# Kernel tuning notes

Hardware: AMD Instinct MI355X
Metric: run time of the kernel (lower is better)

Reference implementation:

```python
import jax, jax.numpy as jnp
import numpy as np

K_T, K_H, K_W = 3, 3, 3
STRIDE = (1, 1, 1)
PAD = (1, 1, 1)
DIL = (1, 1, 1)


def setup_inputs() -> dict:
    key = jax.random.key(0)
    k1, k2, k3, k4 = jax.random.split(key, 4)
    B, C, T, H, W = 2, 16, 8, 64, 64
    Co = 16
    K = K_T * K_H * K_W  # 27
    x = jax.random.normal(k1, (B, C, T, H, W), jnp.float32)
    temp = jax.random.normal(k2, (B, 2 * K, T, H, W), jnp.float32)
    weight = jax.random.normal(k3, (Co, C, K_T, K_H, K_W), jnp.float32) * 0.05
    bias = jax.random.normal(k4, (Co,), jnp.float32) * 0.05
    return {"x": x, "temp": temp, "weight": weight, "bias": bias}


def _build_offset_hw(temp):
    # dimension='HW': per kernel location, offset = (0, temp[2i], temp[2i+1])
    B, c2, T, H, W = temp.shape
    K = c2 // 2
    t = temp.reshape(B, K, 2, T, H, W)
    zeros = jnp.zeros((B, K, 1, T, H, W), temp.dtype)
    return jnp.concatenate([zeros, t], axis=2)  # [B, K, 3, T, H, W]


def _deform_conv3d(x, off, weight, bias):
    # x: [B,C,T,H,W]; off: [B,K,3,To,Ho,Wo]; weight: [Co,C,kT,kH,kW]
    B, C, T, H, W = x.shape
    Co = weight.shape[0]
    K = K_T * K_H * K_W
    st, sh, sw = STRIDE
    pt, ph, pw = PAD
    dt, dh, dw = DIL
    To = (T + 2 * pt - dt * (K_T - 1) - 1) // st + 1
    Ho = (H + 2 * ph - dh * (K_H - 1) - 1) // sh + 1
    Wo = (W + 2 * pw - dw * (K_W - 1) - 1) // sw + 1
    # kernel tap coordinates, flattened to [K]
    kt, kh, kw = jnp.meshgrid(jnp.arange(K_T) * dt, jnp.arange(K_H) * dh,
                              jnp.arange(K_W) * dw, indexing='ij')
    kt, kh, kw = kt.ravel(), kh.ravel(), kw.ravel()
    # base sampling grid (top-left-front corner of receptive field)
    bt = (jnp.arange(To) * st - pt).astype(x.dtype)
    bh = (jnp.arange(Ho) * sh - ph).astype(x.dtype)
    bw = (jnp.arange(Wo) * sw - pw).astype(x.dtype)
    # fractional sampling positions, each [B,K,To,Ho,Wo]
    p_t = bt[None, None, :, None, None] + kt[None, :, None, None, None].astype(x.dtype) + off[:, :, 0]
    p_h = bh[None, None, None, :, None] + kh[None, :, None, None, None].astype(x.dtype) + off[:, :, 1]
    p_w = bw[None, None, None, None, :] + kw[None, :, None, None, None].astype(x.dtype) + off[:, :, 2]
    t0 = jnp.floor(p_t); h0 = jnp.floor(p_h); w0 = jnp.floor(p_w)
    ft = p_t - t0; fh = p_h - h0; fw = p_w - w0
    t0 = t0.astype(jnp.int32); h0 = h0.astype(jnp.int32); w0 = w0.astype(jnp.int32)
    x_flat = x.reshape(B, C, T * H * W)

    def gather_one(xf, idx):  # xf: [C, THW], idx: [K,To,Ho,Wo]
        return xf[:, idx.ravel()].reshape((C,) + idx.shape)

    gather = jax.vmap(gather_one)  # over batch

    val = jnp.zeros((B, C, K, To, Ho, Wo), x.dtype)
    for ot in (0, 1):
        wt = ft if ot else (1.0 - ft)
        ti = t0 + ot
        for oh in (0, 1):
            wh = fh if oh else (1.0 - fh)
            hi = h0 + oh
            for ow in (0, 1):
                ww = fw if ow else (1.0 - fw)
                wi = w0 + ow
                valid = ((ti >= 0) & (ti < T) & (hi >= 0) & (hi < H)
                         & (wi >= 0) & (wi < W))
                idx = (jnp.clip(ti, 0, T - 1) * (H * W)
                       + jnp.clip(hi, 0, H - 1) * W
                       + jnp.clip(wi, 0, W - 1))
                g = gather(x_flat, idx)  # [B,C,K,To,Ho,Wo]
                coef = (wt * wh * ww) * valid.astype(x.dtype)
                val = val + g * coef[:, None]
    w2 = weight.reshape(Co, C, K)
    out = jnp.einsum('bcktuv,ock->botuv', val, w2)
    return out + bias[None, :, None, None, None]


def reference(x, temp, weight, bias):
    off = _build_offset_hw(temp)
    return _deform_conv3d(x, off, weight, bias)
```

## Files before the change

### kernel.cpp

```cpp
#include <hip/hip_runtime.h>

#define BB 2
#define CC 16
#define TT 8
#define HH 64
#define WW 64
#define CO 16
#define KK 27
#define THW (TT*HH*WW)
#define HW  (HH*WW)

typedef _Float16 h8   __attribute__((ext_vector_type(8)));
typedef _Float16 h16  __attribute__((ext_vector_type(16)));
typedef int      i4   __attribute__((ext_vector_type(4)));
typedef float    f32x2 __attribute__((ext_vector_type(2)));

__global__ __launch_bounds__(256) void prep(const float* __restrict__ x,
                                            const float* __restrict__ w,
                                            _Float16* __restrict__ xT,
                                            float* __restrict__ wT) {
    int bid = blockIdx.x;
    if (bid < 256) {
        int pos = bid * 256 + threadIdx.x;
        int b = pos / THW;
        int s = pos - b * THW;
        h16 hv;
#pragma unroll
        for (int c = 0; c < CC; ++c)
            hv[c] = (_Float16)x[(size_t)(b * CC + c) * THW + s];
        *(h16*)(xT + (size_t)pos * CC) = hv;
    } else {
        int id = (bid - 256) * 256 + threadIdx.x;
        if (id < KK * CC * CO) {
            int k  = id / (CC * CO);
            int c  = (id / CO) % CC;
            int co = id % CO;
            wT[id] = w[(size_t)(co * CC + c) * KK + k];
        }
    }
}

template <int CTRL>
__device__ __forceinline__ h8 dppq(h8 v) {
    i4 sv = __builtin_bit_cast(i4, v);
    i4 d;
#pragma unroll
    for (int j = 0; j < 4; ++j)
        d[j] = __builtin_amdgcn_mov_dpp(sv[j], CTRL, 0xF, 0xF, true);
    return __builtin_bit_cast(h8, d);
}

__global__ __launch_bounds__(512, 4) void deform_pair(
    const _Float16* __restrict__ xT, const float* __restrict__ temp,
    const float* __restrict__ wT, const float* __restrict__ bias,
    float* __restrict__ out)
{
    __shared__ float red[4 * CO * 64];

    int tid = threadIdx.x;
    int e   = tid & 1;
    int wl  = (tid >> 1) & 31;
    int wh  = __builtin_amdgcn_readfirstlane((tid >> 6) & 1);
    int g   = __builtin_amdgcn_readfirstlane(tid >> 7);
    int w   = wh * 32 + wl;
    int s0  = blockIdx.x * 64;
    int b   = s0 / THW;
    int sb  = s0 - b * THW;
    int t   = sb / HW;
    int h   = (sb - t * HW) >> 6;

    const float* tb = temp + (size_t)b * (2 * KK) * THW + sb + w;
    float offh[7], offw[7];
#pragma unroll
    for (int i = 0; i < 7; ++i) {
        int k = g + 4 * i;
        if (k < KK) {
            offh[i] = tb[(size_t)(2 * k)     * THW];
            offw[i] = tb[(size_t)(2 * k + 1) * THW];
        }
    }

    f32x2 acc2[8];
#pragma unroll
    for (int j = 0; j < 8; ++j) acc2[j] = f32x2{0.f, 0.f};

#pragma unroll
    for (int i = 0; i < 7; ++i) {
        int k = g + 4 * i;
        if (k >= KK) continue;
        int kt = k / 9, kh = (k / 3) % 3, kw = k % 3;
        int pt = t - 1 + kt;
        if (pt < 0 || pt >= TT) continue;

        float ph = (float)(h - 1 + kh) + offh[i];
        float pw = (float)(w - 1 + kw) + offw[i];
        float r0f = floorf(ph), w0f = floorf(pw);
        float fh = ph - r0f, fw = pw - w0f;
        int r0 = (int)r0f, w0i = (int)w0f;
        int r1 = r0 + 1, w1i = w0i + 1;
        bool vh0 = (unsigned)r0  < (unsigned)HH;
        bool vh1 = (unsigned)r1  < (unsigned)HH;
        bool vw0 = (unsigned)w0i < (unsigned)WW;
        bool vw1 = (unsigned)w1i < (unsigned)WW;
        float fh1 = 1.f - fh, fw1 = 1.f - fw;
        float c00 = fh1 * fw1 * ((vh0 && vw0) ? 1.f : 0.f);
        float c01 = fh1 * fw  * ((vh0 && vw1) ? 1.f : 0.f);
        float c10 = fh  * fw1 * ((vh1 && vw0) ? 1.f : 0.f);
        float c11 = fh  * fw  * ((vh1 && vw1) ? 1.f : 0.f);
        int cc0 = min(max(w0i, 0), WW - 1);
        int cc1 = min(max(w1i, 0), WW - 1);
        int rr0 = min(max(r0, 0), HH - 1);
        int rr1 = min(max(r1, 0), HH - 1);

        const _Float16* xb = xT + (size_t)((b * TT + pt) * HW) * CC + e * 8;
        h8 q00 = *(const h8*)(xb + (size_t)(rr0 * WW + cc0) * CC);
        h8 q01 = *(const h8*)(xb + (size_t)(rr0 * WW + cc1) * CC);
        h8 q10 = *(const h8*)(xb + (size_t)(rr1 * WW + cc0) * CC);
        h8 q11 = *(const h8*)(xb + (size_t)(rr1 * WW + cc1) * CC);

        h8 va = q00 * (_Float16)c00 + q01 * (_Float16)c01
              + q10 * (_Float16)c10 + q11 * (_Float16)c11;

        h8 vlow  = dppq<0xA0>(va);
        h8 vhigh = dppq<0xF5>(va);

        const f32x2* wk = (const f32x2*)(wT + k * (CC * CO));
#pragma unroll
        for (int c = 0; c < 8; ++c) {
            float vl = (float)vlow[c];
            float vh = (float)vhigh[c];
#pragma unroll
            for (int jj = 0; jj < 8; ++jj) {
                acc2[jj] += wk[c * 8 + jj] * vl;
                acc2[jj] += wk[(c + 8) * 8 + jj] * vh;
            }
        }
    }

    if (e == 0) {
#pragma unroll
        for (int j = 0; j < 8; ++j) {
            red[g * (CO * 64) + (2 * j)     * 64 + w] = acc2[j][0];
            red[g * (CO * 64) + (2 * j + 1) * 64 + w] = acc2[j][1];
        }
    }
    __syncthreads();

#pragma unroll
    for (int rep = 0; rep < 2; ++rep) {
        int idx = tid + rep * 512;
        int co = idx >> 6, pp = idx & 63;
        float sum = red[             co * 64 + pp]
                  + red[1 * CO * 64 + co * 64 + pp]
                  + red[2 * CO * 64 + co * 64 + pp]
                  + red[3 * CO * 64 + co * 64 + pp] + bias[co];
        out[(size_t)b * CO * THW + (size_t)co * THW + sb + pp] = sum;
    }
}

__global__ __launch_bounds__(256) void deform_global(
    const float* __restrict__ x, const float* __restrict__ temp,
    const float* __restrict__ weight, const float* __restrict__ bias,
    float* __restrict__ out)
{
    int pos = blockIdx.x * 256 + threadIdx.x;
    int b = pos / THW, s = pos - b * THW;
    int t = s / HW, hw = s - t * HW, h = hw >> 6, w = hw & 63;
    float acc[CO];
#pragma unroll
    for (int co = 0; co < CO; ++co) acc[co] = bias[co];
#pragma unroll 1
    for (int k = 0; k < KK; ++k) {
        int kt = k / 9, kh = (k / 3) % 3, kw = k % 3;
        int pt = t - 1 + kt;
        if (pt < 0 || pt >= TT) continue;
        const float* tb = temp + (size_t)b * (2 * KK) * THW + s;
        float ph = (float)(h - 1 + kh) + tb[(size_t)(2 * k) * THW];
        float pw = (float)(w - 1 + kw) + tb[(size_t)(2 * k + 1) * THW];
        float h0f = floorf(ph), w0f = floorf(pw);
        float fh = ph - h0f, fw = pw - w0f;
        int h0 = (int)h0f, w0 = (int)w0f;
        float val[CC];
#pragma unroll
        for (int c = 0; c < CC; ++c) val[c] = 0.f;
#pragma unroll
        for (int dh = 0; dh < 2; ++dh) {
            int hi = h0 + dh;
            float whf = dh ? fh : (1.f - fh);
            bool vh = (hi >= 0) && (hi < HH);
            int hic = min(max(hi, 0), HH - 1);
#pragma unroll
            for (int dw_ = 0; dw_ < 2; ++dw_) {
                int wi = w0 + dw_;
                float wwf = dw_ ? fw : (1.f - fw);
                bool vw = (wi >= 0) && (wi < WW);
                int wic = min(max(wi, 0), WW - 1);
                float coef = whf * wwf * ((vh && vw) ? 1.f : 0.f);
                const float* xp = x + (size_t)(b * CC) * THW + pt * HW
                                + hic * WW + wic;
#pragma unroll
                for (int c = 0; c < CC; ++c)
                    val[c] = fmaf(coef, xp[(size_t)c * THW], val[c]);
            }
        }
#pragma unroll
        for (int c = 0; c < CC; ++c)
#pragma unroll
            for (int co = 0; co < CO; ++co)
                acc[co] = fmaf(val[c], weight[(size_t)(co * CC + c) * KK + k],
                               acc[co]);
    }
#pragma unroll
    for (int co = 0; co < CO; ++co)
        out[(size_t)(b * CO + co) * THW + s] = acc[co];
}

extern "C" void kernel_launch(void* const* d_in, const int* in_sizes, int n_in,
                              void* d_out, int out_size, void* d_ws, size_t ws_size,
                              hipStream_t stream) {
    const float* x      = (const float*)d_in[0];
    const float* temp   = (const float*)d_in[1];
    const float* weight = (const float*)d_in[2];
    const float* bias   = (const float*)d_in[3];
    float* out = (float*)d_out;

    const size_t xT_bytes = (size_t)BB * THW * CC * sizeof(_Float16);
    const size_t wT_bytes = (size_t)KK * CC * CO * sizeof(float);

    if (ws_size >= xT_bytes + wT_bytes) {
        _Float16* xT = (_Float16*)d_ws;
        float*    wT = (float*)((char*)d_ws + xT_bytes);
        hipLaunchKernelGGL(prep, dim3(256 + 27), dim3(256), 0, stream,
                           x, weight, xT, wT);
        hipLaunchKernelGGL(deform_pair, dim3((BB * THW) / 64), dim3(512),
                           0, stream, xT, temp, wT, bias, out);
    } else {
        hipLaunchKernelGGL(deform_global, dim3((BB * THW) / 256), dim3(256),
                           0, stream, x, temp, weight, bias, out);
    }
}
```

Baseline: 97.80 us.

## Stage input halo tile in swizzled LDS for bilinear gathers

Each block now handles two output rows and first loads a 3-frame by 13-row halo of the fp16 channels-last input into shared memory, using an XOR swizzle to reduce bank conflicts. The four bilinear corner reads then come from LDS, with a rare global fallback when an offset lands outside the staged rows. Each thread now reads all 16 channels itself, so the DPP lane exchange between thread pairs is gone. The aim is to replace scattered global/L2 gathers with LDS reads, at the cost of about 78KB of LDS per block, which limits occupancy, plus extra staging work.

```diff
diff --git a/kernel.cpp b/kernel.cpp
--- a/kernel.cpp
+++ b/kernel.cpp
@@ -12,8 +12,11 @@
 
 typedef _Float16 h8   __attribute__((ext_vector_type(8)));
 typedef _Float16 h16  __attribute__((ext_vector_type(16)));
-typedef int      i4   __attribute__((ext_vector_type(4)));
 typedef float    f32x2 __attribute__((ext_vector_type(2)));
+
+#define NROW 13
+#define ROWB 2048
+#define TILEB (3 * NROW * ROWB)
 
 __global__ __launch_bounds__(256) void prep(const float* __restrict__ x,
                                             const float* __restrict__ w,
@@ -40,36 +43,36 @@
     }
 }
 
-template <int CTRL>
-__device__ __forceinline__ h8 dppq(h8 v) {
-    i4 sv = __builtin_bit_cast(i4, v);
-    i4 d;
-#pragma unroll
-    for (int j = 0; j < 4; ++j)
-        d[j] = __builtin_amdgcn_mov_dpp(sv[j], CTRL, 0xF, 0xF, true);
-    return __builtin_bit_cast(h8, d);
-}
-
-__global__ __launch_bounds__(512, 4) void deform_pair(
+__device__ __forceinline__ int swz(int rr, int c, int base) {
+    int sw = ((((c >> 2) ^ rr) & 3) << 4) | (((c >> 4) & 1) << 6);
+    return base ^ sw;
+}
+
+__global__ __launch_bounds__(512, 4) void deform_lds2(
     const _Float16* __restrict__ xT, const float* __restrict__ temp,
     const float* __restrict__ wT, const float* __restrict__ bias,
     float* __restrict__ out)
 {
-    __shared__ float red[4 * CO * 64];
+    __shared__ __align__(16) char lds[TILEB];
 
     int tid = threadIdx.x;
-    int e   = tid & 1;
-    int wl  = (tid >> 1) & 31;
-    int wh  = __builtin_amdgcn_readfirstlane((tid >> 6) & 1);
-    int g   = __builtin_amdgcn_readfirstlane(tid >> 7);
-    int w   = wh * 32 + wl;
-    int s0  = blockIdx.x * 64;
-    int b   = s0 / THW;
-    int sb  = s0 - b * THW;
-    int t   = sb / HW;
-    int h   = (sb - t * HW) >> 6;
-
-    const float* tb = temp + (size_t)b * (2 * KK) * THW + sb + w;
+    int lane = tid & 63;
+    int wid  = __builtin_amdgcn_readfirstlane(tid >> 6);
+    int row  = wid >> 2;
+    int g    = wid & 3;
+    int blk = blockIdx.x;
+    int b   = blk >> 8;
+    int rem = blk & 255;
+    int t   = rem >> 5;
+    int h0  = (rem & 31) * 2;
+    int rlo = max(0, h0 - 5);
+    int rhi = min(HH - 1, h0 + 7);
+
+    int h = h0 + row;
+    int w = lane;
+    const float* tb = temp + (size_t)b * (2 * KK) * THW
+                    + (size_t)t * HW + h * WW + w;
+
     float offh[7], offw[7];
 #pragma unroll
     for (int i = 0; i < 7; ++i) {
@@ -79,6 +82,28 @@
             offw[i] = tb[(size_t)(2 * k + 1) * THW];
         }
     }
+
+    {
+        const int nchunk = 3 * NROW * 128;
+#pragma unroll
+        for (int it = 0; it < 10; ++it) {
+            int chunk = tid + it * 512;
+            if (chunk >= nchunk) break;
+            int kt  = chunk / (NROW * 128);
+            int r2  = chunk - kt * (NROW * 128);
+            int rr  = r2 >> 7;
+            int j   = r2 & 127;
+            int pt  = t - 1 + kt;
+            int r   = rlo + rr;
+            if (pt >= 0 && pt < TT && r <= rhi) {
+                const h8* src = (const h8*)(xT +
+                    (size_t)((b * TT + pt) * HW + r * WW) * CC) + j;
+                int dst = kt * (NROW * ROWB) + rr * ROWB + j * 16;
+                *(h8*)(lds + swz(rr, j >> 1, dst)) = *src;
+            }
+        }
+    }
+    __syncthreads();
 
     f32x2 acc2[8];
 #pragma unroll
@@ -109,26 +134,47 @@
         float c11 = fh  * fw  * ((vh1 && vw1) ? 1.f : 0.f);
         int cc0 = min(max(w0i, 0), WW - 1);
         int cc1 = min(max(w1i, 0), WW - 1);
-        int rr0 = min(max(r0, 0), HH - 1);
-        int rr1 = min(max(r1, 0), HH - 1);
-
-        const _Float16* xb = xT + (size_t)((b * TT + pt) * HW) * CC + e * 8;
-        h8 q00 = *(const h8*)(xb + (size_t)(rr0 * WW + cc0) * CC);
-        h8 q01 = *(const h8*)(xb + (size_t)(rr0 * WW + cc1) * CC);
-        h8 q10 = *(const h8*)(xb + (size_t)(rr1 * WW + cc0) * CC);
-        h8 q11 = *(const h8*)(xb + (size_t)(rr1 * WW + cc1) * CC);
-
-        h8 va = q00 * (_Float16)c00 + q01 * (_Float16)c01
-              + q10 * (_Float16)c10 + q11 * (_Float16)c11;
-
-        h8 vlow  = dppq<0xA0>(va);
-        h8 vhigh = dppq<0xF5>(va);
+        int rr0 = min(max(r0, rlo), rhi) - rlo;
+        int rr1 = min(max(r1, rlo), rhi) - rlo;
+        int pb = kt * (NROW * ROWB);
+
+        h8 q00a = *(const h8*)(lds + swz(rr0, cc0, pb + rr0 * ROWB + cc0 * 32));
+        h8 q00b = *(const h8*)(lds + swz(rr0, cc0, pb + rr0 * ROWB + cc0 * 32 + 16));
+        h8 q01a = *(const h8*)(lds + swz(rr0, cc1, pb + rr0 * ROWB + cc1 * 32));
+        h8 q01b = *(const h8*)(lds + swz(rr0, cc1, pb + rr0 * ROWB + cc1 * 32 + 16));
+        h8 q10a = *(const h8*)(lds + swz(rr1, cc0, pb + rr1 * ROWB + cc0 * 32));
+        h8 q10b = *(const h8*)(lds + swz(rr1, cc0, pb + rr1 * ROWB + cc0 * 32 + 16));
+        h8 q11a = *(const h8*)(lds + swz(rr1, cc1, pb + rr1 * ROWB + cc1 * 32));
+        h8 q11b = *(const h8*)(lds + swz(rr1, cc1, pb + rr1 * ROWB + cc1 * 32 + 16));
+
+        bool ob0 = vh0 && (r0 < rlo || r0 > rhi);
+        bool ob1 = vh1 && (r1 < rlo || r1 > rhi);
+        if (__builtin_expect(__any(ob0 || ob1), 0)) {
+            const h8* xg = (const h8*)(xT + (size_t)((b * TT + pt) * HW) * CC);
+            if (ob0) {
+                q00a = xg[(r0 * WW + cc0) * 2];
+                q00b = xg[(r0 * WW + cc0) * 2 + 1];
+                q01a = xg[(r0 * WW + cc1) * 2];
+                q01b = xg[(r0 * WW + cc1) * 2 + 1];
+            }
+            if (ob1) {
+                q10a = xg[(r1 * WW + cc0) * 2];
+                q10b = xg[(r1 * WW + cc0) * 2 + 1];
+                q11a = xg[(r1 * WW + cc1) * 2];
+                q11b = xg[(r1 * WW + cc1) * 2 + 1];
+            }
+        }
+
+        _Float16 h00 = (_Float16)c00, h01 = (_Float16)c01;
+        _Float16 h10 = (_Float16)c10, h11 = (_Float16)c11;
+        h8 va = q00a * h00 + q01a * h01 + q10a * h10 + q11a * h11;
+        h8 vb = q00b * h00 + q01b * h01 + q10b * h10 + q11b * h11;
 
         const f32x2* wk = (const f32x2*)(wT + k * (CC * CO));
 #pragma unroll
         for (int c = 0; c < 8; ++c) {
-            float vl = (float)vlow[c];
-            float vh = (float)vhigh[c];
+            float vl = (float)va[c];
+            float vh = (float)vb[c];
 #pragma unroll
             for (int jj = 0; jj < 8; ++jj) {
                 acc2[jj] += wk[c * 8 + jj] * vl;
@@ -137,24 +183,27 @@
         }
     }
 
-    if (e == 0) {
-#pragma unroll
-        for (int j = 0; j < 8; ++j) {
-            red[g * (CO * 64) + (2 * j)     * 64 + w] = acc2[j][0];
-            red[g * (CO * 64) + (2 * j + 1) * 64 + w] = acc2[j][1];
-        }
-    }
     __syncthreads();
-
-#pragma unroll
-    for (int rep = 0; rep < 2; ++rep) {
-        int idx = tid + rep * 512;
-        int co = idx >> 6, pp = idx & 63;
-        float sum = red[             co * 64 + pp]
-                  + red[1 * CO * 64 + co * 64 + pp]
-                  + red[2 * CO * 64 + co * 64 + pp]
-                  + red[3 * CO * 64 + co * 64 + pp] + bias[co];
-        out[(size_t)b * CO * THW + (size_t)co * THW + sb + pp] = sum;
+    float* red = (float*)lds;
+#pragma unroll
+    for (int jj = 0; jj < 8; ++jj) {
+        red[((row * 4 + g) * CO + 2 * jj)     * 64 + w] = acc2[jj][0];
+        red[((row * 4 + g) * CO + 2 * jj + 1) * 64 + w] = acc2[jj][1];
+    }
+    __syncthreads();
+
+#pragma unroll
+    for (int it = 0; it < 4; ++it) {
+        int idx = tid + it * 512;
+        int row2 = idx >> 10;
+        int co   = (idx >> 6) & 15;
+        int p    = idx & 63;
+        float sum = bias[co];
+#pragma unroll
+        for (int gg = 0; gg < 4; ++gg)
+            sum += red[((row2 * 4 + gg) * CO + co) * 64 + p];
+        out[(size_t)b * CO * THW + (size_t)co * THW
+            + t * HW + (h0 + row2) * WW + p] = sum;
     }
 }
 
@@ -232,7 +281,7 @@
         float*    wT = (float*)((char*)d_ws + xT_bytes);
         hipLaunchKernelGGL(prep, dim3(256 + 27), dim3(256), 0, stream,
                            x, weight, xT, wT);
-        hipLaunchKernelGGL(deform_pair, dim3((BB * THW) / 64), dim3(512),
+        hipLaunchKernelGGL(deform_lds2, dim3(BB * TT * (HH / 2)), dim3(512),
                            0, stream, xT, temp, wT, bias, out);
     } else {
         hipLaunchKernelGGL(deform_global, dim3((BB * THW) / 256), dim3(256),
```

New measurement: 91.20 us. -6.8%, faster.
